# Kernel optimization log

Hardware: AMD Instinct MI355X
Metric: run time of the kernel (lower is better)

The kernel has to match this reference:

```python
import jax, jax.numpy as jnp
import numpy as np

BS, SLEN, DIM, N_HEADS = 2, 2048, 2048, 16
DH = DIM // N_HEADS


def setup_inputs() -> dict:
    key = jax.random.key(0)
    ks = jax.random.split(key, 10)
    s = DIM ** -0.5
    x = jax.random.normal(ks[0], (BS, SLEN, DIM), dtype=jnp.float32)
    # causal attention mask from get_masks: True = attend
    mask = jnp.tril(jnp.ones((SLEN, SLEN), dtype=bool))[None].repeat(BS, axis=0)
    Wq = jax.random.normal(ks[1], (DIM, DIM), jnp.float32) * s
    bq = jnp.zeros((DIM,), jnp.float32)
    Wk = jax.random.normal(ks[2], (DIM, DIM), jnp.float32) * s
    bk = jnp.zeros((DIM,), jnp.float32)
    Wv = jax.random.normal(ks[3], (DIM, DIM), jnp.float32) * s
    bv = jnp.zeros((DIM,), jnp.float32)
    Wo = jax.random.normal(ks[4], (DIM, DIM), jnp.float32) * s
    bo = jnp.zeros((DIM,), jnp.float32)
    # normalized_attention learned scalar, init 1/sqrt(dim_per_head)
    scale = jnp.asarray(1.0 / np.sqrt(DH), dtype=jnp.float32)
    return {"x": x, "mask": mask, "Wq": Wq, "bq": bq, "Wk": Wk, "bk": bk,
            "Wv": Wv, "bv": bv, "Wo": Wo, "bo": bo, "scale": scale}


def _split_heads(t):  # (bs, slen, dim) -> (bs, H, slen, dh)
    return t.reshape(BS, -1, N_HEADS, DH).transpose(0, 2, 1, 3)


def reference(x, mask, Wq, bq, Wk, bk, Wv, bv, Wo, bo, scale):
    # QKV projections (torch Linear: x @ W.T + b)
    q = _split_heads(x @ Wq.T + bq)
    k = _split_heads(x @ Wk.T + bk)
    v = _split_heads(x @ Wv.T + bv)
    # normalized attention: L2-normalize q, k on head dim, learned scalar scale
    q = q / jnp.linalg.norm(q, axis=-1, keepdims=True)
    k = k / jnp.linalg.norm(k, axis=-1, keepdims=True)
    q = q * scale
    scores = jnp.einsum('bhqd,bhkd->bhqk', q, k)  # (bs, H, qlen, klen)
    scores = jnp.where(mask[:, None, :, :], scores, -jnp.inf)
    weights = jax.nn.softmax(scores, axis=-1)  # dropout p=0 / eval
    ctx = jnp.einsum('bhqk,bhkd->bhqd', weights, v)
    ctx = ctx.transpose(0, 2, 1, 3).reshape(BS, SLEN, DIM)
    return ctx @ Wo.T + bo
```

## Files before the change

### kernel.cpp

```cpp
#include <hip/hip_runtime.h>
#include <hip/hip_bf16.h>

#define S_LEN 2048
#define DIMN  2048
#define NHEAD 16
#define DHEAD 128
#define SEGQ  ((size_t)4096 * 2048)
#define SEGW  ((size_t)2048 * 2048)

typedef __attribute__((ext_vector_type(8))) short short8;
typedef __attribute__((ext_vector_type(4))) float floatx4;

__device__ inline float bf2f(unsigned short u) {
    union { unsigned int i; float f; } v; v.i = ((unsigned int)u) << 16; return v.f;
}
__device__ inline unsigned short f2bf(float f) {
    unsigned int x = __float_as_uint(f);
    unsigned int r = (x + 0x7FFFu + ((x >> 16) & 1u)) >> 16;
    return (unsigned short)r;
}
__device__ inline short8 ld8_f32_as_bf16(const float* p) {
    float4 a = *(const float4*)p;
    float4 b = *(const float4*)(p + 4);
    short8 r;
    r[0] = (short)f2bf(a.x); r[1] = (short)f2bf(a.y);
    r[2] = (short)f2bf(a.z); r[3] = (short)f2bf(a.w);
    r[4] = (short)f2bf(b.x); r[5] = (short)f2bf(b.y);
    r[6] = (short)f2bf(b.z); r[7] = (short)f2bf(b.w);
    return r;
}
__device__ inline void glds16(unsigned short* lds, const unsigned short* g) {
    __builtin_amdgcn_global_load_lds(
        (const __attribute__((address_space(1))) unsigned int*)g,
        (__attribute__((address_space(3))) unsigned int*)lds, 16, 0, 0);
}

__global__ __launch_bounds__(256) void cvt5_kernel(
    const float* __restrict__ s0, const float* __restrict__ s1,
    const float* __restrict__ s2, const float* __restrict__ s3,
    const float* __restrict__ s4,
    unsigned short* __restrict__ d0, unsigned short* __restrict__ d1,
    unsigned short* __restrict__ d2, unsigned short* __restrict__ d3,
    unsigned short* __restrict__ d4)
{
    const float* s; unsigned short* d; size_t n;
    switch (blockIdx.y) {
        case 0:  s = s0; d = d0; n = SEGQ; break;
        case 1:  s = s1; d = d1; n = SEGW; break;
        case 2:  s = s2; d = d2; n = SEGW; break;
        case 3:  s = s3; d = d3; n = SEGW; break;
        default: s = s4; d = d4; n = SEGW; break;
    }
    size_t stride = (size_t)gridDim.x * 256 * 8;
    for (size_t i = ((size_t)blockIdx.x * 256 + threadIdx.x) * 8; i < n; i += stride)
        *(short8*)&d[i] = ld8_f32_as_bf16(&s[i]);
}

template <int EPI>
__global__ __launch_bounds__(256) void gemm_glds(
    const unsigned short* __restrict__ A, const unsigned short* __restrict__ Bw,
    const float* __restrict__ b0, const float* __restrict__ b1,
    const float* __restrict__ b2, void* __restrict__ Cp,
    int M, int N, int K)
{
    __shared__ __align__(16) unsigned short sA[128 * 32];
    __shared__ __align__(16) unsigned short sB[128 * 32];

    const int tid  = threadIdx.x;
    const int w    = tid >> 6, lane = tid & 63;
    const int l15  = lane & 15, quad = lane >> 4;
    const int wm   = w >> 1, wn = w & 1;
    const int tm   = blockIdx.y * 128, tn = blockIdx.x * 128;
    const int lrow = lane >> 2;
    const int kcol = (lane & 3) * 8;

    floatx4 acc[4][4] = {};

    for (int k0 = 0; k0 < K; k0 += 32) {
        __syncthreads();
#pragma unroll
        for (int i = 0; i < 2; i++) {
            int r0 = w * 32 + i * 16;
            glds16(&sA[r0 * 32], &A[(size_t)(tm + r0 + lrow) * K + k0 + kcol]);
            glds16(&sB[r0 * 32], &Bw[(size_t)(tn + r0 + lrow) * K + k0 + kcol]);
        }
        __syncthreads();

        short8 af[4], bfr[4];
#pragma unroll
        for (int mi = 0; mi < 4; mi++)
            af[mi] = *(const short8*)&sA[(wm * 64 + mi * 16 + l15) * 32 + quad * 8];
#pragma unroll
        for (int ni = 0; ni < 4; ni++)
            bfr[ni] = *(const short8*)&sB[(wn * 64 + ni * 16 + l15) * 32 + quad * 8];
#pragma unroll
        for (int mi = 0; mi < 4; mi++)
#pragma unroll
            for (int ni = 0; ni < 4; ni++)
                acc[mi][ni] = __builtin_amdgcn_mfma_f32_16x16x32_bf16(af[mi], bfr[ni], acc[mi][ni], 0, 0, 0);
    }

#pragma unroll
    for (int mi = 0; mi < 4; mi++) {
        int mbase = tm + wm * 64 + mi * 16 + quad * 4;
#pragma unroll
        for (int ni = 0; ni < 4; ni++) {
            int n = tn + wn * 64 + ni * 16 + l15;
            if (EPI == 0) {
                int t = n >> 11, h = (n >> 7) & 15, dh = n & 127;
                const float* bp = (t == 0) ? b0 : (t == 1) ? b1 : b2;
                float bias = bp[n & 2047];
                unsigned short* Q = (unsigned short*)Cp;
#pragma unroll
                for (int r = 0; r < 4; r++) {
                    int m = mbase + r;
                    int b = m >> 11, s = m & 2047;
                    float v = acc[mi][ni][r] + bias;
                    size_t idx = (t < 2)
                        ? (size_t)t * SEGQ + (((size_t)(b * NHEAD + h)) * S_LEN + s) * DHEAD + dh
                        : 2 * SEGQ + (((size_t)(b * NHEAD + h)) * DHEAD + dh) * S_LEN + s;
                    Q[idx] = f2bf(v);
                }
            } else {
                float bias = b0[n];
#pragma unroll
                for (int r = 0; r < 4; r++) {
                    int m = mbase + r;
                    ((float*)Cp)[(size_t)m * N + n] = acc[mi][ni][r] + bias;
                }
            }
        }
    }
}

template <int SPLIT, int A_F32, int OUT_F32>
__global__ __launch_bounds__(256) void gemm_bt(
    const void* __restrict__ Ap, const float* __restrict__ Bw,
    const float* __restrict__ bias, void* __restrict__ Cp,
    int M, int N, int K)
{
    __shared__ __align__(16) unsigned short sA[128 * 40];
    __shared__ __align__(16) unsigned short sB[128 * 40];

    const int tid  = threadIdx.x;
    const int w    = tid >> 6, lane = tid & 63;
    const int l15  = lane & 15, quad = lane >> 4;
    const int wm   = w >> 1, wn = w & 1;
    const int tm   = blockIdx.y * 128, tn = blockIdx.x * 128;

    const float*          Af32 = (const float*)Ap;
    const unsigned short* Abf  = (const unsigned short*)Ap;

    floatx4 acc[4][4] = {};

    for (int k0 = 0; k0 < K; k0 += 32) {
        __syncthreads();
#pragma unroll
        for (int i = 0; i < 2; i++) {
            int c   = tid + i * 256;
            int row = c >> 2;
            int kc  = (c & 3) * 8;
            size_t goff = (size_t)(tm + row) * K + k0 + kc;
            if (A_F32)
                *(short8*)&sA[row * 40 + kc] = ld8_f32_as_bf16(&Af32[goff]);
            else
                *(short8*)&sA[row * 40 + kc] = *(const short8*)&Abf[goff];
            *(short8*)&sB[row * 40 + kc] =
                ld8_f32_as_bf16(&Bw[(size_t)(tn + row) * K + k0 + kc]);
        }
        __syncthreads();

        short8 af[4], bfr[4];
#pragma unroll
        for (int mi = 0; mi < 4; mi++)
            af[mi] = *(const short8*)&sA[(wm * 64 + mi * 16 + l15) * 40 + quad * 8];
#pragma unroll
        for (int ni = 0; ni < 4; ni++)
            bfr[ni] = *(const short8*)&sB[(wn * 64 + ni * 16 + l15) * 40 + quad * 8];
#pragma unroll
        for (int mi = 0; mi < 4; mi++)
#pragma unroll
            for (int ni = 0; ni < 4; ni++)
                acc[mi][ni] = __builtin_amdgcn_mfma_f32_16x16x32_bf16(af[mi], bfr[ni], acc[mi][ni], 0, 0, 0);
    }

#pragma unroll
    for (int mi = 0; mi < 4; mi++) {
        int mbase = tm + wm * 64 + mi * 16 + quad * 4;
#pragma unroll
        for (int ni = 0; ni < 4; ni++) {
            int n = tn + wn * 64 + ni * 16 + l15;
            float bv = bias[n];
#pragma unroll
            for (int r = 0; r < 4; r++) {
                int m = mbase + r;
                float v = acc[mi][ni][r] + bv;
                if (SPLIT == 1) {
                    int b = m >> 11, s = m & 2047, h = n >> 7, dh = n & 127;
                    ((unsigned short*)Cp)[(((size_t)(b * NHEAD + h)) * S_LEN + s) * DHEAD + dh] = f2bf(v);
                } else if (SPLIT == 2) {
                    int b = m >> 11, s = m & 2047, h = n >> 7, dh = n & 127;
                    ((unsigned short*)Cp)[(((size_t)(b * NHEAD + h)) * DHEAD + dh) * S_LEN + s] = f2bf(v);
                } else if (OUT_F32) {
                    ((float*)Cp)[(size_t)m * N + n] = v;
                } else {
                    ((unsigned short*)Cp)[(size_t)m * N + n] = f2bf(v);
                }
            }
        }
    }
}

__global__ __launch_bounds__(256) void l2norm_kernel(
    unsigned short* __restrict__ qn, unsigned short* __restrict__ kn,
    const float* __restrict__ scale_p)
{
    const int w = threadIdx.x >> 6, lane = threadIdx.x & 63;
    size_t row = (size_t)blockIdx.x * 4 + w;
    unsigned short* base = (blockIdx.y == 0 ? qn : kn) + row * DHEAD;
    float a = bf2f(base[lane * 2]);
    float b = bf2f(base[lane * 2 + 1]);
    float ss = a * a + b * b;
#pragma unroll
    for (int off = 1; off < 64; off <<= 1) ss += __shfl_xor(ss, off, 64);
    float f = rsqrtf(ss);
    if (blockIdx.y == 0) f *= scale_p[0];
    base[lane * 2]     = f2bf(a * f);
    base[lane * 2 + 1] = f2bf(b * f);
}

#define KSTR  136
#define VTSTR 72
#define PSTR  72

__global__ __launch_bounds__(256) void attn_kernel3(
    const unsigned short* __restrict__ qn, const unsigned short* __restrict__ kn,
    const unsigned short* __restrict__ vt, unsigned short* __restrict__ ctx)
{
    __shared__ __align__(16) unsigned short sK [64 * KSTR];
    __shared__ __align__(16) unsigned short sVt[DHEAD * VTSTR];
    __shared__ __align__(16) unsigned short sP [4 * 16 * PSTR];

    const int tid  = threadIdx.x;
    const int w    = tid >> 6, lane = tid & 63;
    const int l15  = lane & 15, quad = lane >> 4;
    const int xb   = blockIdx.x, bh = blockIdx.y;
    const size_t headoff = (size_t)bh * S_LEN * DHEAD;
    const unsigned short* kbase0 = kn + headoff;
    const unsigned short* vtbase = vt + headoff;
    unsigned short* sPw = sP + w * 16 * PSTR;

    const int vrow = tid >> 1, vhalf = (tid & 1) * 32;

    short8 kpre[4], vpre[4];

    for (int half = 0; half < 2; half++) {
        const int qt = half ? (31 - xb) : xb;

        const unsigned short* qrow = qn + headoff + (size_t)(qt * 64 + w * 16 + l15) * DHEAD;
        short8 aQ[4];
#pragma unroll
        for (int ks = 0; ks < 4; ks++) aQ[ks] = *(const short8*)(qrow + ks * 32 + quad * 8);

        floatx4 O[8] = {};
        float m_i[4], l_i[4];
#pragma unroll
        for (int r = 0; r < 4; r++) { m_i[r] = -1e30f; l_i[r] = 0.0f; }

        if (half == 0) {
#pragma unroll
            for (int j = 0; j < 4; j++) {
                int c = tid + j * 256;
                kpre[j] = *(const short8*)(kbase0 + (size_t)(c >> 4) * DHEAD + (c & 15) * 8);
            }
#pragma unroll
            for (int j = 0; j < 4; j++)
                vpre[j] = *(const short8*)(vtbase + (size_t)vrow * S_LEN + vhalf + j * 8);
        }

        for (int kt = 0; kt <= qt; kt++) {
            __syncthreads();

#pragma unroll
            for (int j = 0; j < 4; j++) {
                int c = tid + j * 256;
                *(short8*)&sK[(c >> 4) * KSTR + (c & 15) * 8] = kpre[j];
            }
#pragma unroll
            for (int j = 0; j < 4; j++)
                *(short8*)&sVt[vrow * VTSTR + vhalf + j * 8] = vpre[j];

            if (kt < qt || half == 0) {
                const int knext = (kt < qt) ? (kt + 1) * 64 : 0;
#pragma unroll
                for (int j = 0; j < 4; j++) {
                    int c = tid + j * 256;
                    kpre[j] = *(const short8*)(kbase0 + (size_t)knext * DHEAD + (size_t)(c >> 4) * DHEAD + (c & 15) * 8);
                }
#pragma unroll
                for (int j = 0; j < 4; j++)
                    vpre[j] = *(const short8*)(vtbase + (size_t)vrow * S_LEN + knext + vhalf + j * 8);
            }
            __syncthreads();

            floatx4 sc[4] = {};
#pragma unroll
            for (int ks = 0; ks < 4; ks++) {
#pragma unroll
                for (int ni = 0; ni < 4; ni++) {
                    short8 bK = *(const short8*)&sK[(ni * 16 + l15) * KSTR + ks * 32 + quad * 8];
                    sc[ni] = __builtin_amdgcn_mfma_f32_16x16x32_bf16(aQ[ks], bK, sc[ni], 0, 0, 0);
                }
            }

            if (kt == qt) {
#pragma unroll
                for (int ni = 0; ni < 4; ni++) {
                    int cl = ni * 16 + l15;
#pragma unroll
                    for (int r = 0; r < 4; r++) {
                        int rl = w * 16 + quad * 4 + r;
                        if (cl > rl) sc[ni][r] = -1e30f;
                    }
                }
            }

            float rmax[4];
#pragma unroll
            for (int r = 0; r < 4; r++)
                rmax[r] = fmaxf(fmaxf(sc[0][r], sc[1][r]), fmaxf(sc[2][r], sc[3][r]));
#pragma unroll
            for (int off = 1; off < 16; off <<= 1)
#pragma unroll
                for (int r = 0; r < 4; r++) rmax[r] = fmaxf(rmax[r], __shfl_xor(rmax[r], off, 64));

            float alpha[4], rsum[4];
#pragma unroll
            for (int r = 0; r < 4; r++) {
                float mn = fmaxf(m_i[r], rmax[r]);
                alpha[r] = exp2f((m_i[r] - mn) * 1.44269504f);
                m_i[r] = mn;
                rsum[r] = 0.0f;
            }
#pragma unroll
            for (int ni = 0; ni < 4; ni++) {
#pragma unroll
                for (int r = 0; r < 4; r++) {
                    float p = exp2f((sc[ni][r] - m_i[r]) * 1.44269504f);
                    rsum[r] += p;
                    sPw[(quad * 4 + r) * PSTR + ni * 16 + l15] = f2bf(p);
                }
            }
#pragma unroll
            for (int off = 1; off < 16; off <<= 1)
#pragma unroll
                for (int r = 0; r < 4; r++) rsum[r] += __shfl_xor(rsum[r], off, 64);
#pragma unroll
            for (int r = 0; r < 4; r++) l_i[r] = l_i[r] * alpha[r] + rsum[r];
#pragma unroll
            for (int t = 0; t < 8; t++)
#pragma unroll
                for (int r = 0; r < 4; r++) O[t][r] *= alpha[r];

            __syncthreads();

#pragma unroll
            for (int ks2 = 0; ks2 < 2; ks2++) {
                short8 aP = *(const short8*)&sPw[l15 * PSTR + ks2 * 32 + quad * 8];
#pragma unroll
                for (int t = 0; t < 8; t++) {
                    short8 bV = *(const short8*)&sVt[(t * 16 + l15) * VTSTR + ks2 * 32 + quad * 8];
                    O[t] = __builtin_amdgcn_mfma_f32_16x16x32_bf16(aP, bV, O[t], 0, 0, 0);
                }
            }
        }

        const int b = bh >> 4, h = bh & 15;
#pragma unroll
        for (int r = 0; r < 4; r++) {
            float inv = 1.0f / l_i[r];
            int srow = qt * 64 + w * 16 + quad * 4 + r;
            size_t rowoff = ((size_t)(b * S_LEN + srow)) * DIMN + h * DHEAD;
#pragma unroll
            for (int t = 0; t < 8; t++)
                ctx[rowoff + t * 16 + l15] = f2bf(O[t][r] * inv);
        }
    }
}

extern "C" void kernel_launch(void* const* d_in, const int* in_sizes, int n_in,
                              void* d_out, int out_size, void* d_ws, size_t ws_size,
                              hipStream_t stream)
{
    const float* x     = (const float*)d_in[0];
    const float* Wq    = (const float*)d_in[2];
    const float* bq    = (const float*)d_in[3];
    const float* Wk    = (const float*)d_in[4];
    const float* bk    = (const float*)d_in[5];
    const float* Wv    = (const float*)d_in[6];
    const float* bv    = (const float*)d_in[7];
    const float* Wo    = (const float*)d_in[8];
    const float* bo    = (const float*)d_in[9];
    const float* scale = (const float*)d_in[10];

    const int M = 4096, N = 2048, K = 2048;
    float* out = (float*)d_out;
    const size_t need = (SEGQ + 4 * SEGW + 3 * SEGQ) * sizeof(unsigned short);

    if (ws_size >= need) {
        unsigned short* xb  = (unsigned short*)d_ws;
        unsigned short* wqb = xb  + SEGQ;
        unsigned short* wkb = wqb + SEGW;
        unsigned short* wvb = wkb + SEGW;
        unsigned short* wob = wvb + SEGW;
        unsigned short* qn  = wob + SEGW;
        unsigned short* kn  = qn  + SEGQ;
        unsigned short* vtb = kn  + SEGQ;
        unsigned short* ctx = xb;

        cvt5_kernel<<<dim3(512, 5), 256, 0, stream>>>(x, Wq, Wk, Wv, Wo,
                                                      xb, wqb, wkb, wvb, wob);
        gemm_glds<0><<<dim3(48, 32), 256, 0, stream>>>(xb, wqb, bq, bk, bv, qn, M, 6144, K);
        l2norm_kernel<<<dim3(16384, 2), 256, 0, stream>>>(qn, kn, scale);
        attn_kernel3<<<dim3(16, 32), 256, 0, stream>>>(qn, kn, vtb, ctx);
        gemm_glds<1><<<dim3(16, 32), 256, 0, stream>>>(ctx, wob, bo, nullptr, nullptr, out, M, N, K);
    } else {
        unsigned short* qn  = (unsigned short*)d_ws;
        unsigned short* kn  = qn + SEGQ;
        unsigned short* vtb = kn + SEGQ;
        unsigned short* ctx = vtb + SEGQ;

        gemm_bt<1, 1, 0><<<dim3(16, 32), 256, 0, stream>>>(x, Wq, bq, qn, M, N, K);
        gemm_bt<1, 1, 0><<<dim3(16, 32), 256, 0, stream>>>(x, Wk, bk, kn, M, N, K);
        gemm_bt<2, 1, 0><<<dim3(16, 32), 256, 0, stream>>>(x, Wv, bv, vtb, M, N, K);
        l2norm_kernel<<<dim3(16384, 2), 256, 0, stream>>>(qn, kn, scale);
        attn_kernel3<<<dim3(16, 32), 256, 0, stream>>>(qn, kn, vtb, ctx);
        gemm_bt<0, 0, 1><<<dim3(16, 32), 256, 0, stream>>>(ctx, Wo, bo, out, M, N, K);
    }
}
```

Baseline: 500.2 us.

## Fuse L2-norm into QKV GEMM epilogue and enlarge attention tiles to 128

The QKV projection epilogue now computes per-row sums of squares across each 128-wide head tile, combining the two wave halves through shared memory. It applies rsqrt and the learned scale before storing, which removes the separate l2norm pass that re-read and rewrote Q and K. The attention kernel is widened to 512 threads with 128-row Q and K tiles, doubling per-block reuse of K and V loads and halving the grid to 256 blocks. The trade-offs are more LDS and registers per block and fewer blocks to balance the causal workload. Normalisation now happens before rounding to bf16 rather than after, which slightly changes numerics.

After: 462.5 us. 7.5% less time.

```diff
diff --git a/kernel.cpp b/kernel.cpp
--- a/kernel.cpp
+++ b/kernel.cpp
@@ -60,8 +60,8 @@
 __global__ __launch_bounds__(256) void gemm_glds(
     const unsigned short* __restrict__ A, const unsigned short* __restrict__ Bw,
     const float* __restrict__ b0, const float* __restrict__ b1,
-    const float* __restrict__ b2, void* __restrict__ Cp,
-    int M, int N, int K)
+    const float* __restrict__ b2, const float* __restrict__ scale_p,
+    void* __restrict__ Cp, int M, int N, int K)
 {
     __shared__ __align__(16) unsigned short sA[128 * 32];
     __shared__ __align__(16) unsigned short sB[128 * 32];
@@ -100,28 +100,70 @@
                 acc[mi][ni] = __builtin_amdgcn_mfma_f32_16x16x32_bf16(af[mi], bfr[ni], acc[mi][ni], 0, 0, 0);
     }
 
-#pragma unroll
-    for (int mi = 0; mi < 4; mi++) {
-        int mbase = tm + wm * 64 + mi * 16 + quad * 4;
+    if (EPI == 0) {
+        const int t = tn >> 11;
+        const float* bp = (t == 0) ? b0 : (t == 1) ? b1 : b2;
+        unsigned short* Q = (unsigned short*)Cp;
 #pragma unroll
         for (int ni = 0; ni < 4; ni++) {
             int n = tn + wn * 64 + ni * 16 + l15;
-            if (EPI == 0) {
-                int t = n >> 11, h = (n >> 7) & 15, dh = n & 127;
-                const float* bp = (t == 0) ? b0 : (t == 1) ? b1 : b2;
-                float bias = bp[n & 2047];
-                unsigned short* Q = (unsigned short*)Cp;
-#pragma unroll
-                for (int r = 0; r < 4; r++) {
-                    int m = mbase + r;
-                    int b = m >> 11, s = m & 2047;
-                    float v = acc[mi][ni][r] + bias;
+            float bias = bp[n & 2047];
+#pragma unroll
+            for (int mi = 0; mi < 4; mi++)
+#pragma unroll
+                for (int r = 0; r < 4; r++) acc[mi][ni][r] += bias;
+        }
+        float ssq[4][4];
+#pragma unroll
+        for (int mi = 0; mi < 4; mi++)
+#pragma unroll
+            for (int r = 0; r < 4; r++) {
+                float s = 0.0f;
+#pragma unroll
+                for (int ni = 0; ni < 4; ni++) s += acc[mi][ni][r] * acc[mi][ni][r];
+#pragma unroll
+                for (int off = 1; off < 16; off <<= 1) s += __shfl_xor(s, off, 64);
+                ssq[mi][r] = s;
+            }
+        __syncthreads();
+        float* ssh = (float*)sA;
+        if (l15 == 0) {
+#pragma unroll
+            for (int mi = 0; mi < 4; mi++)
+#pragma unroll
+                for (int r = 0; r < 4; r++)
+                    ssh[wn * 128 + wm * 64 + mi * 16 + quad * 4 + r] = ssq[mi][r];
+        }
+        __syncthreads();
+        const float scl = (t == 0) ? scale_p[0] : 1.0f;
+#pragma unroll
+        for (int mi = 0; mi < 4; mi++) {
+            int mbase = tm + wm * 64 + mi * 16 + quad * 4;
+#pragma unroll
+            for (int r = 0; r < 4; r++) {
+                float tot = ssq[mi][r] + ssh[(wn ^ 1) * 128 + wm * 64 + mi * 16 + quad * 4 + r];
+                float f = (t < 2) ? rsqrtf(tot) * scl : 1.0f;
+                int m = mbase + r;
+                int b = m >> 11, s = m & 2047;
+#pragma unroll
+                for (int ni = 0; ni < 4; ni++) {
+                    int n = tn + wn * 64 + ni * 16 + l15;
+                    int h = (n >> 7) & 15, dh = n & 127;
+                    float v = acc[mi][ni][r] * f;
                     size_t idx = (t < 2)
                         ? (size_t)t * SEGQ + (((size_t)(b * NHEAD + h)) * S_LEN + s) * DHEAD + dh
                         : 2 * SEGQ + (((size_t)(b * NHEAD + h)) * DHEAD + dh) * S_LEN + s;
                     Q[idx] = f2bf(v);
                 }
-            } else {
+            }
+        }
+    } else {
+#pragma unroll
+        for (int mi = 0; mi < 4; mi++) {
+            int mbase = tm + wm * 64 + mi * 16 + quad * 4;
+#pragma unroll
+            for (int ni = 0; ni < 4; ni++) {
+                int n = tn + wn * 64 + ni * 16 + l15;
                 float bias = b0[n];
 #pragma unroll
                 for (int r = 0; r < 4; r++) {
@@ -230,16 +272,16 @@
 }
 
 #define KSTR  136
-#define VTSTR 72
-#define PSTR  72
-
-__global__ __launch_bounds__(256) void attn_kernel3(
+#define VTSTR 136
+#define PSTR  136
+
+__global__ __launch_bounds__(512) void attn_kernel4(
     const unsigned short* __restrict__ qn, const unsigned short* __restrict__ kn,
     const unsigned short* __restrict__ vt, unsigned short* __restrict__ ctx)
 {
-    __shared__ __align__(16) unsigned short sK [64 * KSTR];
-    __shared__ __align__(16) unsigned short sVt[DHEAD * VTSTR];
-    __shared__ __align__(16) unsigned short sP [4 * 16 * PSTR];
+    __shared__ __align__(16) unsigned short sK [128 * KSTR];
+    __shared__ __align__(16) unsigned short sVt[128 * VTSTR];
+    __shared__ __align__(16) unsigned short sP [8 * 16 * PSTR];
 
     const int tid  = threadIdx.x;
     const int w    = tid >> 6, lane = tid & 63;
@@ -250,14 +292,12 @@
     const unsigned short* vtbase = vt + headoff;
     unsigned short* sPw = sP + w * 16 * PSTR;
 
-    const int vrow = tid >> 1, vhalf = (tid & 1) * 32;
-
     short8 kpre[4], vpre[4];
 
     for (int half = 0; half < 2; half++) {
-        const int qt = half ? (31 - xb) : xb;
-
-        const unsigned short* qrow = qn + headoff + (size_t)(qt * 64 + w * 16 + l15) * DHEAD;
+        const int qt = half ? (15 - xb) : xb;
+
+        const unsigned short* qrow = qn + headoff + (size_t)(qt * 128 + w * 16 + l15) * DHEAD;
         short8 aQ[4];
 #pragma unroll
         for (int ks = 0; ks < 4; ks++) aQ[ks] = *(const short8*)(qrow + ks * 32 + quad * 8);
@@ -270,12 +310,10 @@
         if (half == 0) {
 #pragma unroll
             for (int j = 0; j < 4; j++) {
-                int c = tid + j * 256;
+                int c = tid + j * 512;
                 kpre[j] = *(const short8*)(kbase0 + (size_t)(c >> 4) * DHEAD + (c & 15) * 8);
-            }
-#pragma unroll
-            for (int j = 0; j < 4; j++)
-                vpre[j] = *(const short8*)(vtbase + (size_t)vrow * S_LEN + vhalf + j * 8);
+                vpre[j] = *(const short8*)(vtbase + (size_t)(c >> 4) * S_LEN + (c & 15) * 8);
+            }
         }
 
         for (int kt = 0; kt <= qt; kt++) {
@@ -283,31 +321,27 @@
 
 #pragma unroll
             for (int j = 0; j < 4; j++) {
-                int c = tid + j * 256;
-                *(short8*)&sK[(c >> 4) * KSTR + (c & 15) * 8] = kpre[j];
-            }
-#pragma unroll
-            for (int j = 0; j < 4; j++)
-                *(short8*)&sVt[vrow * VTSTR + vhalf + j * 8] = vpre[j];
+                int c = tid + j * 512;
+                *(short8*)&sK [(c >> 4) * KSTR  + (c & 15) * 8] = kpre[j];
+                *(short8*)&sVt[(c >> 4) * VTSTR + (c & 15) * 8] = vpre[j];
+            }
 
             if (kt < qt || half == 0) {
-                const int knext = (kt < qt) ? (kt + 1) * 64 : 0;
+                const int knext = (kt < qt) ? (kt + 1) * 128 : 0;
 #pragma unroll
                 for (int j = 0; j < 4; j++) {
-                    int c = tid + j * 256;
-                    kpre[j] = *(const short8*)(kbase0 + (size_t)knext * DHEAD + (size_t)(c >> 4) * DHEAD + (c & 15) * 8);
-                }
-#pragma unroll
-                for (int j = 0; j < 4; j++)
-                    vpre[j] = *(const short8*)(vtbase + (size_t)vrow * S_LEN + knext + vhalf + j * 8);
+                    int c = tid + j * 512;
+                    kpre[j] = *(const short8*)(kbase0 + (size_t)(knext + (c >> 4)) * DHEAD + (c & 15) * 8);
+                    vpre[j] = *(const short8*)(vtbase + (size_t)(c >> 4) * S_LEN + knext + (c & 15) * 8);
+                }
             }
             __syncthreads();
 
-            floatx4 sc[4] = {};
+            floatx4 sc[8] = {};
 #pragma unroll
             for (int ks = 0; ks < 4; ks++) {
 #pragma unroll
-                for (int ni = 0; ni < 4; ni++) {
+                for (int ni = 0; ni < 8; ni++) {
                     short8 bK = *(const short8*)&sK[(ni * 16 + l15) * KSTR + ks * 32 + quad * 8];
                     sc[ni] = __builtin_amdgcn_mfma_f32_16x16x32_bf16(aQ[ks], bK, sc[ni], 0, 0, 0);
                 }
@@ -315,7 +349,7 @@
 
             if (kt == qt) {
 #pragma unroll
-                for (int ni = 0; ni < 4; ni++) {
+                for (int ni = 0; ni < 8; ni++) {
                     int cl = ni * 16 + l15;
 #pragma unroll
                     for (int r = 0; r < 4; r++) {
@@ -327,8 +361,12 @@
 
             float rmax[4];
 #pragma unroll
-            for (int r = 0; r < 4; r++)
-                rmax[r] = fmaxf(fmaxf(sc[0][r], sc[1][r]), fmaxf(sc[2][r], sc[3][r]));
+            for (int r = 0; r < 4; r++) {
+                float mx = sc[0][r];
+#pragma unroll
+                for (int ni = 1; ni < 8; ni++) mx = fmaxf(mx, sc[ni][r]);
+                rmax[r] = mx;
+            }
 #pragma unroll
             for (int off = 1; off < 16; off <<= 1)
 #pragma unroll
@@ -343,7 +381,7 @@
                 rsum[r] = 0.0f;
             }
 #pragma unroll
-            for (int ni = 0; ni < 4; ni++) {
+            for (int ni = 0; ni < 8; ni++) {
 #pragma unroll
                 for (int r = 0; r < 4; r++) {
                     float p = exp2f((sc[ni][r] - m_i[r]) * 1.44269504f);
@@ -365,7 +403,7 @@
             __syncthreads();
 
 #pragma unroll
-            for (int ks2 = 0; ks2 < 2; ks2++) {
+            for (int ks2 = 0; ks2 < 4; ks2++) {
                 short8 aP = *(const short8*)&sPw[l15 * PSTR + ks2 * 32 + quad * 8];
 #pragma unroll
                 for (int t = 0; t < 8; t++) {
@@ -379,7 +417,7 @@
 #pragma unroll
         for (int r = 0; r < 4; r++) {
             float inv = 1.0f / l_i[r];
-            int srow = qt * 64 + w * 16 + quad * 4 + r;
+            int srow = qt * 128 + w * 16 + quad * 4 + r;
             size_t rowoff = ((size_t)(b * S_LEN + srow)) * DIMN + h * DHEAD;
 #pragma unroll
             for (int t = 0; t < 8; t++)
@@ -420,10 +458,9 @@
 
         cvt5_kernel<<<dim3(512, 5), 256, 0, stream>>>(x, Wq, Wk, Wv, Wo,
                                                       xb, wqb, wkb, wvb, wob);
-        gemm_glds<0><<<dim3(48, 32), 256, 0, stream>>>(xb, wqb, bq, bk, bv, qn, M, 6144, K);
-        l2norm_kernel<<<dim3(16384, 2), 256, 0, stream>>>(qn, kn, scale);
-        attn_kernel3<<<dim3(16, 32), 256, 0, stream>>>(qn, kn, vtb, ctx);
-        gemm_glds<1><<<dim3(16, 32), 256, 0, stream>>>(ctx, wob, bo, nullptr, nullptr, out, M, N, K);
+        gemm_glds<0><<<dim3(48, 32), 256, 0, stream>>>(xb, wqb, bq, bk, bv, scale, qn, M, 6144, K);
+        attn_kernel4<<<dim3(8, 32), 512, 0, stream>>>(qn, kn, vtb, ctx);
+        gemm_glds<1><<<dim3(16, 32), 256, 0, stream>>>(ctx, wob, bo, nullptr, nullptr, nullptr, out, M, N, K);
     } else {
         unsigned short* qn  = (unsigned short*)d_ws;
         unsigned short* kn  = qn + SEGQ;
@@ -434,7 +471,7 @@
         gemm_bt<1, 1, 0><<<dim3(16, 32), 256, 0, stream>>>(x, Wk, bk, kn, M, N, K);
         gemm_bt<2, 1, 0><<<dim3(16, 32), 256, 0, stream>>>(x, Wv, bv, vtb, M, N, K);
         l2norm_kernel<<<dim3(16384, 2), 256, 0, stream>>>(qn, kn, scale);
-        attn_kernel3<<<dim3(16, 32), 256, 0, stream>>>(qn, kn, vtb, ctx);
+        attn_kernel4<<<dim3(8, 32), 512, 0, stream>>>(qn, kn, vtb, ctx);
         gemm_bt<0, 0, 1><<<dim3(16, 32), 256, 0, stream>>>(ctx, Wo, bo, out, M, N, K);
     }
 }
```
